# Kernel tuning notes

Hardware: AMD Instinct MI355X
Metric: run time of the kernel (lower is better)

## Reference

```python
import jax, jax.numpy as jnp
import numpy as np

N_SHARD = 4
PPP = 512            # positive_per_partition
NEG = 1024           # padded_negative
E = 256              # embedding size
N_ENT = 250000       # entities per shard (local table)
N_REL = 1000


def setup_inputs() -> dict:
    key = jax.random.key(0)
    k1, k2, k3, k4, k5, k6 = jax.random.split(key, 6)
    return {
        "head": jax.random.randint(k1, (N_SHARD, PPP), 0, N_ENT),
        "relation": jax.random.randint(k2, (N_SHARD, PPP), 0, N_REL),
        "tail": jax.random.randint(k3, (N_SHARD, PPP), 0, N_ENT),
        "negative": jax.random.randint(k4, (N_SHARD, 1, NEG), 0, N_ENT),
        "entity_embedding": jax.random.normal(k5, (N_ENT, E), dtype=jnp.float32),
        "relation_embedding": jax.random.normal(k6, (N_REL, E), dtype=jnp.float32),
    }


def reference(head, relation, tail, negative, entity_embedding, relation_embedding):
    n_shard, ppp = head.shape
    emb_size = entity_embedding.shape[-1]

    # --- phase 1: gather local embeddings (single fused gather, as in the module) ---
    negative_flat = negative.reshape(n_shard, -1)                       # (S, NEG)
    gather_idx = jnp.concatenate([head, tail, negative_flat], axis=1)   # (S, 2*ppp+NEG)
    emb = entity_embedding[gather_idx]                                  # (S, 2*ppp+NEG, E)
    head_embedding = emb[:, :ppp]                                       # (S, ppp, E)
    tail_embedding = emb[:, ppp:2 * ppp]                                # (S, ppp, E)
    negative_embedding = emb[:, 2 * ppp:].reshape(*negative.shape, emb_size)  # (S,1,NEG,E)
    # flat negative format: single shared negative set
    negative_embedding = negative_embedding[0][None]                    # (1, 1, NEG, E)

    # --- phase 2: collectives (simulated on replicated data) ---
    # all_gather -> new leading n_shard dim
    relation_all = jnp.broadcast_to(relation, (n_shard, n_shard, ppp))  # (S, S, ppp)
    # corruption scheme 't': all_gather head embeddings
    head_embedding_all = jnp.broadcast_to(
        head_embedding, (n_shard, n_shard, ppp, emb_size))              # (S, S, ppp, E)

    # --- phase 3: scoring (DistMult, negative sample sharing) ---
    h = head_embedding_all.reshape(-1, emb_size)                        # (S*S*ppp, E)
    r = relation_embedding[relation_all.reshape(-1)]                    # (S*S*ppp, E)
    t_neg = negative_embedding.reshape(-1, emb_size)                    # (NEG, E)
    negative_score = jnp.einsum('ne,me->nm', h * r, t_neg)             # (S*S*ppp, NEG)

    # route scores back: reshape -> all_to_all (identity on replicated data)
    # -> transpose -> flatten, exactly as in the module
    negative_score = negative_score.reshape(n_shard, n_shard * ppp, -1)
    negative_score = jnp.transpose(negative_score, (1, 0, 2)).reshape(n_shard * ppp, -1)
    # (S*ppp, S*NEG)

    # tail_embedding = all_to_all(tail_embedding) -> identity in simulation
    hp = head_embedding.reshape(-1, emb_size)
    rp = relation_embedding[relation.reshape(-1)]
    tp = tail_embedding.reshape(-1, emb_size)
    positive_score = jnp.sum(hp * rp * tp, axis=-1)                     # (S*ppp,)

    return positive_score, negative_score
```

## Files before the change

### kernel.cpp

```cpp
#include <hip/hip_runtime.h>
#include <hip/hip_bf16.h>

#define N_SHARD 4
#define PPP     512
#define NEG_N   1024
#define EMB     256
#define NROWS   (N_SHARD * PPP)

typedef __attribute__((ext_vector_type(8))) short bf16x8;
typedef __attribute__((ext_vector_type(4))) float f32x4;

__device__ __forceinline__ unsigned short f2bf(float f) {
    union { float f; unsigned int u; } v; v.f = f;
    return (unsigned short)((v.u + 0x7FFFu + ((v.u >> 16) & 1u)) >> 16);
}

__global__ __launch_bounds__(512, 1) void fused_kernel(
    const int* __restrict__ head, const int* __restrict__ relation,
    const int* __restrict__ tail, const int* __restrict__ negative,
    const float* __restrict__ ent, const float* __restrict__ relemb,
    float* __restrict__ pos_out, float* __restrict__ neg_out)
{
    __shared__ unsigned short Abuf[64 * EMB];
    __shared__ unsigned short Bbuf[128 * EMB];
    __shared__ int idxbuf[64 * 3 + 128];

    const int tid  = threadIdx.x;
    const int wid  = tid >> 6;
    const int lane = tid & 63;
    const int p    = blockIdx.x & 31;
    const int q    = blockIdx.x >> 5;
    const int row0 = p * 64;
    const int colp = q * 128;

    int* hIdx = idxbuf;
    int* rIdx = idxbuf + 64;
    int* tIdx = idxbuf + 128;
    int* nIdx = idxbuf + 192;

    if (tid < 64)            hIdx[tid]       = head[row0 + tid];
    else if (tid < 128)      rIdx[tid - 64]  = relation[row0 + tid - 64];
    else if (tid < 256)      nIdx[tid - 128] = negative[colp + tid - 128];
    else if (tid < 320 && q == 0) tIdx[tid - 256] = tail[row0 + tid - 256];
    __syncthreads();

    #pragma unroll
    for (int i = 0; i < 8; ++i) {
        const int r = wid * 8 + i;
        const float4 h4 = ((const float4*)(ent    + (size_t)hIdx[r] * EMB))[lane];
        const float4 r4 = ((const float4*)(relemb + (size_t)rIdx[r] * EMB))[lane];
        const float x = h4.x * r4.x, y = h4.y * r4.y;
        const float z = h4.z * r4.z, w = h4.w * r4.w;
        const ushort4 s = make_ushort4(f2bf(x), f2bf(y), f2bf(z), f2bf(w));
        *(ushort4*)((char*)Abuf + r * 512 + ((lane * 8) ^ ((r & 7) << 4))) = s;
        if (q == 0) {
            const float4 t4 = ((const float4*)(ent + (size_t)tIdx[r] * EMB))[lane];
            float pd = x * t4.x + y * t4.y + z * t4.z + w * t4.w;
            #pragma unroll
            for (int off = 32; off > 0; off >>= 1) pd += __shfl_down(pd, off, 64);
            if (lane == 0) pos_out[row0 + r] = pd;
        }
    }
    #pragma unroll
    for (int i = 0; i < 16; ++i) {
        const int m = wid * 16 + i;
        const float4 t4 = ((const float4*)(ent + (size_t)nIdx[m] * EMB))[lane];
        const ushort4 s = make_ushort4(f2bf(t4.x), f2bf(t4.y), f2bf(t4.z), f2bf(t4.w));
        *(ushort4*)((char*)Bbuf + m * 512 + ((lane * 8) ^ ((m & 7) << 4))) = s;
    }
    __syncthreads();

    const int r16  = lane & 15;
    const int half = lane >> 4;
    const int wr   = wid >> 1, wc = wid & 1;
    const int arow = wr * 16 + r16;
    const int aswz = (arow & 7) << 4;
    const int bb   = wc * 64;
    const int bswz = (r16 & 7) << 4;

    f32x4 acc[4];
    #pragma unroll
    for (int nf = 0; nf < 4; ++nf) acc[nf] = (f32x4){0.f, 0.f, 0.f, 0.f};

    #pragma unroll
    for (int kk = 0; kk < 8; ++kk) {
        const int koff = kk * 64 + half * 16;
        const bf16x8 a = *(const bf16x8*)((const char*)Abuf + arow * 512 + (koff ^ aswz));
        #pragma unroll
        for (int nf = 0; nf < 4; ++nf) {
            const bf16x8 b = *(const bf16x8*)((const char*)Bbuf + (bb + nf * 16 + r16) * 512 + (koff ^ bswz));
            acc[nf] = __builtin_amdgcn_mfma_f32_16x16x32_bf16(a, b, acc[nf], 0, 0, 0);
        }
    }
    __syncthreads();

    float* cw = (float*)((char*)Abuf + wid * 4096);
    #pragma unroll
    for (int v = 0; v < 4; ++v) {
        const int lr = half * 4 + v;
        #pragma unroll
        for (int nf = 0; nf < 4; ++nf) {
            const int c = nf * 16 + r16;
            cw[lr * 64 + (c ^ (half << 4))] = acc[nf][v];
        }
    }
    #pragma unroll
    for (int j = 0; j < 4; ++j) {
        const int lr = j * 4 + half;
        const f32x4 v4 = *(const f32x4*)&cw[lr * 64 + ((r16 * 4) ^ (j << 4))];
        const int grow = row0 + wr * 16 + lr;
        float* orow = neg_out + (size_t)grow * 4096 + colp + wc * 64 + r16 * 4;
        __builtin_nontemporal_store(v4, (f32x4*)(orow));
        __builtin_nontemporal_store(v4, (f32x4*)(orow + 1024));
        __builtin_nontemporal_store(v4, (f32x4*)(orow + 2048));
        __builtin_nontemporal_store(v4, (f32x4*)(orow + 3072));
    }
}

extern "C" void kernel_launch(void* const* d_in, const int* in_sizes, int n_in,
                              void* d_out, int out_size, void* d_ws, size_t ws_size,
                              hipStream_t stream) {
    const int*   head     = (const int*)d_in[0];
    const int*   relation = (const int*)d_in[1];
    const int*   tail     = (const int*)d_in[2];
    const int*   negative = (const int*)d_in[3];
    const float* ent      = (const float*)d_in[4];
    const float* rel      = (const float*)d_in[5];

    float* pos_out = (float*)d_out;
    float* neg_out = (float*)d_out + NROWS;

    fused_kernel<<<256, 512, 0, stream>>>(head, relation, tail, negative,
                                          ent, rel, pos_out, neg_out);
}
```

Before: 18.16 us.

## Process two column tiles per block, reusing A tile and overlapping B reload

Each block now covers 256 negative columns instead of 128, so the launch drops to 128 blocks. The head-times-relation A tile is gathered once and reused for two B tiles, which halves redundant A gathers. The second B tile's gather is issued before the first tile's epilogue stores, to overlap load latency with output writes. The epilogue gets a dedicated LDS staging buffer for this, which raises shared memory use, and with half as many blocks only about half of the CUs on an MI355X have work.

```diff
diff --git a/kernel.cpp b/kernel.cpp
--- a/kernel.cpp
+++ b/kernel.cpp
@@ -23,25 +23,26 @@
 {
     __shared__ unsigned short Abuf[64 * EMB];
     __shared__ unsigned short Bbuf[128 * EMB];
-    __shared__ int idxbuf[64 * 3 + 128];
+    __shared__ float cwbuf[8 * 1024];
+    __shared__ int idxbuf[448];
 
     const int tid  = threadIdx.x;
     const int wid  = tid >> 6;
     const int lane = tid & 63;
     const int p    = blockIdx.x & 31;
-    const int q    = blockIdx.x >> 5;
+    const int cq   = blockIdx.x >> 5;
     const int row0 = p * 64;
-    const int colp = q * 128;
+    const int colq = cq * 256;
 
     int* hIdx = idxbuf;
     int* rIdx = idxbuf + 64;
-    int* tIdx = idxbuf + 128;
-    int* nIdx = idxbuf + 192;
+    int* nIdx = idxbuf + 128;
+    int* tIdx = idxbuf + 384;
 
-    if (tid < 64)            hIdx[tid]       = head[row0 + tid];
-    else if (tid < 128)      rIdx[tid - 64]  = relation[row0 + tid - 64];
-    else if (tid < 256)      nIdx[tid - 128] = negative[colp + tid - 128];
-    else if (tid < 320 && q == 0) tIdx[tid - 256] = tail[row0 + tid - 256];
+    if (tid < 64)       hIdx[tid]       = head[row0 + tid];
+    else if (tid < 128) rIdx[tid - 64]  = relation[row0 + tid - 64];
+    else if (tid < 384) nIdx[tid - 128] = negative[colq + tid - 128];
+    else if (cq == 0)   tIdx[tid - 384] = tail[row0 + tid - 384];
     __syncthreads();
 
     #pragma unroll
@@ -53,7 +54,7 @@
         const float z = h4.z * r4.z, w = h4.w * r4.w;
         const ushort4 s = make_ushort4(f2bf(x), f2bf(y), f2bf(z), f2bf(w));
         *(ushort4*)((char*)Abuf + r * 512 + ((lane * 8) ^ ((r & 7) << 4))) = s;
-        if (q == 0) {
+        if (cq == 0) {
             const float4 t4 = ((const float4*)(ent + (size_t)tIdx[r] * EMB))[lane];
             float pd = x * t4.x + y * t4.y + z * t4.z + w * t4.w;
             #pragma unroll
@@ -77,6 +78,7 @@
     const int aswz = (arow & 7) << 4;
     const int bb   = wc * 64;
     const int bswz = (r16 & 7) << 4;
+    float* cw = cwbuf + wid * 1024;
 
     f32x4 acc[4];
     #pragma unroll
@@ -94,7 +96,13 @@
     }
     __syncthreads();
 
-    float* cw = (float*)((char*)Abuf + wid * 4096);
+    #pragma unroll
+    for (int i = 0; i < 16; ++i) {
+        const int m = wid * 16 + i;
+        const float4 t4 = ((const float4*)(ent + (size_t)nIdx[128 + m] * EMB))[lane];
+        const ushort4 s = make_ushort4(f2bf(t4.x), f2bf(t4.y), f2bf(t4.z), f2bf(t4.w));
+        *(ushort4*)((char*)Bbuf + m * 512 + ((lane * 8) ^ ((m & 7) << 4))) = s;
+    }
     #pragma unroll
     for (int v = 0; v < 4; ++v) {
         const int lr = half * 4 + v;
@@ -109,7 +117,42 @@
         const int lr = j * 4 + half;
         const f32x4 v4 = *(const f32x4*)&cw[lr * 64 + ((r16 * 4) ^ (j << 4))];
         const int grow = row0 + wr * 16 + lr;
-        float* orow = neg_out + (size_t)grow * 4096 + colp + wc * 64 + r16 * 4;
+        float* orow = neg_out + (size_t)grow * 4096 + colq + bb + r16 * 4;
+        __builtin_nontemporal_store(v4, (f32x4*)(orow));
+        __builtin_nontemporal_store(v4, (f32x4*)(orow + 1024));
+        __builtin_nontemporal_store(v4, (f32x4*)(orow + 2048));
+        __builtin_nontemporal_store(v4, (f32x4*)(orow + 3072));
+    }
+    __syncthreads();
+
+    #pragma unroll
+    for (int nf = 0; nf < 4; ++nf) acc[nf] = (f32x4){0.f, 0.f, 0.f, 0.f};
+    #pragma unroll
+    for (int kk = 0; kk < 8; ++kk) {
+        const int koff = kk * 64 + half * 16;
+        const bf16x8 a = *(const bf16x8*)((const char*)Abuf + arow * 512 + (koff ^ aswz));
+        #pragma unroll
+        for (int nf = 0; nf < 4; ++nf) {
+            const bf16x8 b = *(const bf16x8*)((const char*)Bbuf + (bb + nf * 16 + r16) * 512 + (koff ^ bswz));
+            acc[nf] = __builtin_amdgcn_mfma_f32_16x16x32_bf16(a, b, acc[nf], 0, 0, 0);
+        }
+    }
+
+    #pragma unroll
+    for (int v = 0; v < 4; ++v) {
+        const int lr = half * 4 + v;
+        #pragma unroll
+        for (int nf = 0; nf < 4; ++nf) {
+            const int c = nf * 16 + r16;
+            cw[lr * 64 + (c ^ (half << 4))] = acc[nf][v];
+        }
+    }
+    #pragma unroll
+    for (int j = 0; j < 4; ++j) {
+        const int lr = j * 4 + half;
+        const f32x4 v4 = *(const f32x4*)&cw[lr * 64 + ((r16 * 4) ^ (j << 4))];
+        const int grow = row0 + wr * 16 + lr;
+        float* orow = neg_out + (size_t)grow * 4096 + colq + 128 + bb + r16 * 4;
         __builtin_nontemporal_store(v4, (f32x4*)(orow));
         __builtin_nontemporal_store(v4, (f32x4*)(orow + 1024));
         __builtin_nontemporal_store(v4, (f32x4*)(orow + 2048));
@@ -130,6 +173,6 @@
     float* pos_out = (float*)d_out;
     float* neg_out = (float*)d_out + NROWS;
 
-    fused_kernel<<<256, 512, 0, stream>>>(head, relation, tail, negative,
+    fused_kernel<<<128, 512, 0, stream>>>(head, relation, tail, negative,
                                           ent, rel, pos_out, neg_out);
 }
```

After: 19.35 us. 1.07x slower.
